# Optimization experiments

Hardware: AMD Instinct MI355X
Metric: run time of the kernel (lower is better)

The kernel has to match this reference:

```python
import jax, jax.numpy as jnp
import numpy as np

B, S, D, H = 1, 4096, 1024, 16
HD = D // H  # head_dim = 64
NEG = -1e9

def setup_inputs() -> dict:
    key = jax.random.key(0)
    ks = jax.random.split(key, 5)
    scale = 1.0 / np.sqrt(D)
    x = jax.random.normal(ks[0], (B, S, D), dtype=jnp.float32)
    Wq = jax.random.normal(ks[1], (D, D), dtype=jnp.float32) * scale
    Wk = jax.random.normal(ks[2], (D, D), dtype=jnp.float32) * scale
    Wv = jax.random.normal(ks[3], (D, D), dtype=jnp.float32) * scale
    Wo = jax.random.normal(ks[4], (D, D), dtype=jnp.float32) * scale
    mask = jnp.tril(jnp.ones((S, S), dtype=bool))[None, None]  # [1,1,S,S] causal
    return {"x": x, "mask": mask, "Wq": Wq, "Wk": Wk, "Wv": Wv, "Wo": Wo}

def reference(x, mask, Wq, Wk, Wv, Wo):
    # Linear projections (bias=False). nn.Linear computes x @ W.T; weights here
    # are stored as [out, in] so we use x @ W.T for faithfulness.
    q = x @ Wq.T  # [B,S,D]
    k = x @ Wk.T
    v = x @ Wv.T
    def split_heads(t):
        return t.reshape(B, S, H, HD).transpose(0, 2, 1, 3)  # [B,H,S,HD]
    q, k, v = split_heads(q), split_heads(k), split_heads(v)
    scores = jnp.einsum("bhqd,bhkd->bhqk", q, k) / jnp.sqrt(jnp.float32(HD))
    scores = jnp.where(mask, scores, NEG)
    attn = jax.nn.softmax(scores, axis=-1)  # dropout p=0.0 -> identity
    out = jnp.einsum("bhqk,bhkd->bhqd", attn, v)  # [B,H,S,HD]
    out = out.transpose(0, 2, 1, 3).reshape(B, S, D)
    return out @ Wo.T
```

## Files before the change

### kernel.cpp

```cpp
#include <hip/hip_runtime.h>
#include <hip/hip_bf16.h>


typedef __bf16 bf16x8 __attribute__((ext_vector_type(8)));
typedef __bf16 bf16x4 __attribute__((ext_vector_type(4)));
typedef float f32x4 __attribute__((ext_vector_type(4)));

#define GAS __attribute__((address_space(1)))
#define LAS __attribute__((address_space(3)))

__device__ __forceinline__ void async_copy16(const void* g, void* l) {
  __builtin_amdgcn_global_load_lds((const GAS unsigned int*)g,
                                   (LAS unsigned int*)l, 16, 0, 0);
}

__global__ __launch_bounds__(256) void cvt_all(const float* __restrict__ x,
                                               const float* __restrict__ Wq,
                                               const float* __restrict__ Wk,
                                               const float* __restrict__ Wv,
                                               const float* __restrict__ Wo,
                                               __bf16* __restrict__ xb,
                                               __bf16* __restrict__ Wc,
                                               __bf16* __restrict__ Wob) {
  int b = blockIdx.x;
  const float* src;
  __bf16* dst;
  if (b < 4096)      { src = x  + (b       ) * 1024; dst = xb  + (long)b * 1024; }
  else if (b < 5120) { src = Wq + (b - 4096) * 1024; dst = Wc  + (long)(b - 4096) * 1024; }
  else if (b < 6144) { src = Wk + (b - 5120) * 1024; dst = Wc  + (1l << 20) + (long)(b - 5120) * 1024; }
  else if (b < 7168) { src = Wv + (b - 6144) * 1024; dst = Wc  + (2l << 20) + (long)(b - 6144) * 1024; }
  else               { src = Wo + (b - 7168) * 1024; dst = Wob + (long)(b - 7168) * 1024; }
  int i = threadIdx.x * 4;
  float4 f = *(const float4*)(src + i);
  bf16x4 o;
  o[0] = (__bf16)f.x; o[1] = (__bf16)f.y; o[2] = (__bf16)f.z; o[3] = (__bf16)f.w;
  *(bf16x4*)(dst + i) = o;
}

__global__ __launch_bounds__(256) void gemm_qkv(const __bf16* __restrict__ A,
                                                const __bf16* __restrict__ B,
                                                __bf16* __restrict__ Qb,
                                                __bf16* __restrict__ Kf,
                                                __bf16* __restrict__ Vf) {
  const int K = 1024;
  __shared__ __bf16 As[128 * 32];
  __shared__ __bf16 Bs[128 * 32];
  const int tid = threadIdx.x;
  const int lane = tid & 63, wv = tid >> 6;
  const int l15 = lane & 15, quad = lane >> 4;
  const int wm = wv >> 1, wn = wv & 1;
  const int mbase = blockIdx.y * 128, nbase = blockIdx.x * 128;
  const bool kswap = (nbase >= 1024) && (nbase < 2048);

  f32x4 acc[4][4] = {};

  for (int k0 = 0; k0 < K; k0 += 32) {
    __syncthreads();
#pragma unroll
    for (int q = 0; q < 2; ++q) {
      int i = q * 256 + tid;
      int row = i >> 2, kg = i & 3;
      const __bf16* ga = A + (long)(mbase + row) * K + k0 + kg * 8;
      const __bf16* gb = B + (long)(nbase + row) * K + k0 + kg * 8;
      char* la = (char*)As + (q * 256 + wv * 64) * 16;
      char* lb = (char*)Bs + (q * 256 + wv * 64) * 16;
      async_copy16(ga, la);
      async_copy16(gb, lb);
    }
    __syncthreads();
    bf16x8 af[4], bfr[4];
#pragma unroll
    for (int i = 0; i < 4; ++i)
      af[i] = *(const bf16x8*)&As[(wm * 64 + i * 16 + l15) * 32 + quad * 8];
#pragma unroll
    for (int j = 0; j < 4; ++j)
      bfr[j] = *(const bf16x8*)&Bs[(wn * 64 + j * 16 + l15) * 32 + quad * 8];
    if (kswap) {
#pragma unroll
      for (int i = 0; i < 4; ++i)
#pragma unroll
        for (int j = 0; j < 4; ++j)
          acc[i][j] = __builtin_amdgcn_mfma_f32_16x16x32_bf16(bfr[j], af[i], acc[i][j], 0, 0, 0);
    } else {
#pragma unroll
      for (int i = 0; i < 4; ++i)
#pragma unroll
        for (int j = 0; j < 4; ++j)
          acc[i][j] = __builtin_amdgcn_mfma_f32_16x16x32_bf16(af[i], bfr[j], acc[i][j], 0, 0, 0);
    }
  }

  if (nbase < 1024) {
    const float QS = 0.18033688011112043f;
#pragma unroll
    for (int i = 0; i < 4; ++i)
#pragma unroll
      for (int j = 0; j < 4; ++j) {
        int col = nbase + wn * 64 + j * 16 + l15;
#pragma unroll
        for (int r = 0; r < 4; ++r) {
          int row = mbase + wm * 64 + i * 16 + quad * 4 + r;
          Qb[(long)row * 1024 + col] = (__bf16)(acc[i][j][r] * QS);
        }
      }
  } else if (nbase < 2048) {
#pragma unroll
    for (int i = 0; i < 4; ++i)
#pragma unroll
      for (int j = 0; j < 4; ++j) {
        int d0 = nbase - 1024 + wn * 64 + j * 16 + quad * 4;
        int h = d0 >> 6, dd = d0 & 63;
        int kk = dd >> 5, qf = (dd >> 3) & 3, e0 = dd & 7;
        int kt = mbase + wm * 64 + i * 16 + l15;
        int tile = kt >> 6;
        long off = ((long)(h * 64 + tile) * 8 + i * 2 + kk) * 512 + (qf * 16 + l15) * 8 + e0;
        union { __bf16 b[4]; uint2 u; } pk;
#pragma unroll
        for (int r = 0; r < 4; ++r) pk.b[r] = (__bf16)acc[i][j][r];
        *(uint2*)(Kf + off) = pk.u;
      }
  } else {
#pragma unroll
    for (int i = 0; i < 4; ++i)
#pragma unroll
      for (int j = 0; j < 4; ++j) {
        int col = nbase - 2048 + wn * 64 + j * 16 + l15;
        int h = col >> 6, dd = col & 63;
        int jd = dd >> 4, lv = dd & 15;
        int kt0 = mbase + wm * 64 + i * 16 + quad * 4;
        int tile = kt0 >> 6, w6 = kt0 & 63;
        int t = w6 >> 5, qv = (w6 >> 3) & 3, e0 = w6 & 7;
        long off = ((long)(h * 64 + tile) * 8 + jd * 2 + t) * 512 + (qv * 16 + lv) * 8 + e0;
        union { __bf16 b[4]; uint2 u; } pk;
#pragma unroll
        for (int r = 0; r < 4; ++r) pk.b[r] = (__bf16)acc[i][j][r];
        *(uint2*)(Vf + off) = pk.u;
      }
  }
}

__global__ __launch_bounds__(256) void gemm_wo(const __bf16* __restrict__ A,
                                               const __bf16* __restrict__ B,
                                               float* __restrict__ C) {
  const int K = 1024, N = 1024;
  __shared__ __bf16 As[128 * 32];
  __shared__ __bf16 Bs[64 * 32];
  const int tid = threadIdx.x;
  const int lane = tid & 63, wv = tid >> 6;
  const int l15 = lane & 15, quad = lane >> 4;
  const int wm = wv >> 1, wn = wv & 1;
  const int mbase = blockIdx.y * 128, nbase = blockIdx.x * 64;

  f32x4 acc[4][2] = {};

  for (int k0 = 0; k0 < K; k0 += 32) {
    __syncthreads();
#pragma unroll
    for (int q = 0; q < 2; ++q) {
      int i = q * 256 + tid;
      int row = i >> 2, kg = i & 3;
      const __bf16* ga = A + (long)(mbase + row) * K + k0 + kg * 8;
      char* la = (char*)As + (q * 256 + wv * 64) * 16;
      async_copy16(ga, la);
    }
    {
      int row = tid >> 2, kg = tid & 3;
      const __bf16* gb = B + (long)(nbase + row) * K + k0 + kg * 8;
      char* lb = (char*)Bs + (wv * 64) * 16;
      async_copy16(gb, lb);
    }
    __syncthreads();
    bf16x8 af[4], bfr[2];
#pragma unroll
    for (int i = 0; i < 4; ++i)
      af[i] = *(const bf16x8*)&As[(wm * 64 + i * 16 + l15) * 32 + quad * 8];
#pragma unroll
    for (int j = 0; j < 2; ++j)
      bfr[j] = *(const bf16x8*)&Bs[(wn * 32 + j * 16 + l15) * 32 + quad * 8];
#pragma unroll
    for (int i = 0; i < 4; ++i)
#pragma unroll
      for (int j = 0; j < 2; ++j)
        acc[i][j] = __builtin_amdgcn_mfma_f32_16x16x32_bf16(af[i], bfr[j], acc[i][j], 0, 0, 0);
  }
#pragma unroll
  for (int i = 0; i < 4; ++i)
#pragma unroll
    for (int j = 0; j < 2; ++j)
#pragma unroll
      for (int r = 0; r < 4; ++r) {
        int row = mbase + wm * 64 + i * 16 + quad * 4 + r;
        int col = nbase + wn * 32 + j * 16 + l15;
        C[(long)row * N + col] = acc[i][j][r];
      }
}

__global__ __launch_bounds__(256, 2) void flash_attn(const __bf16* __restrict__ Qb,
                                                     const __bf16* __restrict__ Kf,
                                                     const __bf16* __restrict__ Vf,
                                                     __bf16* __restrict__ AO) {
  __shared__ float Ms[2][64][36];
  const int tid = threadIdx.x;
  const int lane = tid & 63, l15 = lane & 15, quad = lane >> 4;
  const int w = tid >> 6;
  const int u = w >> 1, hf = w & 1;
  const int b = blockIdx.x;
  const int h = (b & 7) + 8 * ((b >> 3) & 1);
  const int T = 63 - (b >> 4);
  const int hoff = h * 64;

  const __bf16* Kh = Kf + (long)h * 64 * 4096;
  const __bf16* Vh = Vf + (long)h * 64 * 4096;

  bf16x8 qf[2][2];
#pragma unroll
  for (int g = 0; g < 2; ++g) {
    const int qrow = T * 64 + u * 32 + g * 16 + l15;
    qf[g][0] = *(const bf16x8*)(Qb + (long)qrow * 1024 + hoff + quad * 8);
    qf[g][1] = *(const bf16x8*)(Qb + (long)qrow * 1024 + hoff + 32 + quad * 8);
  }

  const int nkt = T + 1;
  const int kt0 = hf ? (nkt >> 1) : 0;
  const int kt1 = hf ? nkt : (nkt >> 1);
  f32x4 o_acc[2][4] = {};
  float l_acc[2] = {0.0f, 0.0f};

  bf16x8 kc[8];
  if (kt0 < kt1) {
    const __bf16* Kt = Kh + (long)kt0 * 4096;
#pragma unroll
    for (int f = 0; f < 8; ++f)
      kc[f] = *(const bf16x8*)(Kt + f * 512 + lane * 8);
  }

  for (int kt = kt0; kt < kt1; ++kt) {
    const __bf16* Vt = Vh + (long)kt * 4096;

    f32x4 stg[2][4] = {};
#pragma unroll
    for (int g = 0; g < 2; ++g)
#pragma unroll
      for (int j = 0; j < 4; ++j) {
        stg[g][j] = __builtin_amdgcn_mfma_f32_16x16x32_bf16(kc[j * 2 + 0], qf[g][0], stg[g][j], 0, 0, 0);
        stg[g][j] = __builtin_amdgcn_mfma_f32_16x16x32_bf16(kc[j * 2 + 1], qf[g][1], stg[g][j], 0, 0, 0);
      }

    bf16x8 va0[4];
#pragma unroll
    for (int jd = 0; jd < 4; ++jd)
      va0[jd] = *(const bf16x8*)(Vt + (jd * 2) * 512 + lane * 8);

    if (kt + 1 < kt1) {
      const __bf16* Kt = Kh + (long)(kt + 1) * 4096;
#pragma unroll
      for (int f = 0; f < 8; ++f)
        kc[f] = *(const bf16x8*)(Kt + f * 512 + lane * 8);
    }

    if (kt == nkt - 1) {
#pragma unroll
      for (int g = 0; g < 2; ++g) {
        const int dq = u * 32 + g * 16 + l15;
#pragma unroll
        for (int j = 0; j < 4; ++j)
#pragma unroll
          for (int r = 0; r < 4; ++r)
            if (j * 16 + quad * 4 + r > dq) stg[g][j][r] = -3.0e38f;
      }
    }

    unsigned dj[2][4][2];
#pragma unroll
    for (int g = 0; g < 2; ++g) {
      float ps = 0.0f;
#pragma unroll
      for (int j = 0; j < 4; ++j) {
        f32x4 pj;
#pragma unroll
        for (int r = 0; r < 4; ++r) pj[r] = __builtin_amdgcn_exp2f(stg[g][j][r]);
        ps += (pj[0] + pj[1]) + (pj[2] + pj[3]);
        union { __bf16 h2[2]; unsigned uu; } p0, p1;
        p0.h2[0] = (__bf16)pj[0]; p0.h2[1] = (__bf16)pj[1];
        p1.h2[0] = (__bf16)pj[2]; p1.h2[1] = (__bf16)pj[3];
        dj[g][j][0] = p0.uu;
        dj[g][j][1] = p1.uu;
      }
      l_acc[g] += ps;
    }

    bf16x8 va1[4];
#pragma unroll
    for (int jd = 0; jd < 4; ++jd)
      va1[jd] = *(const bf16x8*)(Vt + (jd * 2 + 1) * 512 + lane * 8);

#pragma unroll
    for (int g = 0; g < 2; ++g) {
      unsigned m0 = dj[g][0][0], m2 = dj[g][1][0];
      unsigned m1 = dj[g][0][1], m3 = dj[g][1][1];
      asm volatile("v_permlane32_swap_b32 %0, %1" : "+v"(m0), "+v"(m2));
      asm volatile("v_permlane32_swap_b32 %0, %1" : "+v"(m1), "+v"(m3));
      asm volatile("v_permlane16_swap_b32 %0, %1" : "+v"(m0), "+v"(m2));
      asm volatile("v_permlane16_swap_b32 %0, %1" : "+v"(m1), "+v"(m3));
      union { unsigned u4[4]; bf16x8 v; } Bf;
      Bf.u4[0] = m0; Bf.u4[1] = m1; Bf.u4[2] = m2; Bf.u4[3] = m3;
#pragma unroll
      for (int jd = 0; jd < 4; ++jd)
        o_acc[g][jd] = __builtin_amdgcn_mfma_f32_16x16x32_bf16(va0[jd], Bf.v, o_acc[g][jd], 0, 0, 0);
    }
#pragma unroll
    for (int g = 0; g < 2; ++g) {
      unsigned m0 = dj[g][2][0], m2 = dj[g][3][0];
      unsigned m1 = dj[g][2][1], m3 = dj[g][3][1];
      asm volatile("v_permlane32_swap_b32 %0, %1" : "+v"(m0), "+v"(m2));
      asm volatile("v_permlane32_swap_b32 %0, %1" : "+v"(m1), "+v"(m3));
      asm volatile("v_permlane16_swap_b32 %0, %1" : "+v"(m0), "+v"(m2));
      asm volatile("v_permlane16_swap_b32 %0, %1" : "+v"(m1), "+v"(m3));
      union { unsigned u4[4]; bf16x8 v; } Bf;
      Bf.u4[0] = m0; Bf.u4[1] = m1; Bf.u4[2] = m2; Bf.u4[3] = m3;
#pragma unroll
      for (int jd = 0; jd < 4; ++jd)
        o_acc[g][jd] = __builtin_amdgcn_mfma_f32_16x16x32_bf16(va1[jd], Bf.v, o_acc[g][jd], 0, 0, 0);
    }
  }

  if (hf) {
#pragma unroll
    for (int g = 0; g < 2; ++g)
#pragma unroll
      for (int jd = 0; jd < 4; ++jd)
        *(f32x4*)&Ms[u][lane][g * 16 + jd * 4] = o_acc[g][jd];
    Ms[u][lane][32] = l_acc[0];
    Ms[u][lane][33] = l_acc[1];
  }
  __syncthreads();
  if (!hf) {
#pragma unroll
    for (int g = 0; g < 2; ++g) {
      float la = l_acc[g];
#pragma unroll
      for (int jd = 0; jd < 4; ++jd)
        o_acc[g][jd] += *(const f32x4*)&Ms[u][lane][g * 16 + jd * 4];
      la += Ms[u][lane][32 + g];
      la += __shfl_xor(la, 16);
      la += __shfl_xor(la, 32);
      const float inv = 1.0f / la;
      const int qrow = T * 64 + u * 32 + g * 16 + l15;
#pragma unroll
      for (int jd = 0; jd < 4; ++jd) {
        bf16x4 ob;
#pragma unroll
        for (int r = 0; r < 4; ++r) ob[r] = (__bf16)(o_acc[g][jd][r] * inv);
        *(bf16x4*)(AO + (long)qrow * 1024 + hoff + jd * 16 + quad * 4) = ob;
      }
    }
  }
}

extern "C" void kernel_launch(void* const* d_in, const int* in_sizes, int n_in,
                              void* d_out, int out_size, void* d_ws, size_t ws_size,
                              hipStream_t stream) {
  const float* x  = (const float*)d_in[0];
  const float* Wq = (const float*)d_in[2];
  const float* Wk = (const float*)d_in[3];
  const float* Wv = (const float*)d_in[4];
  const float* Wo = (const float*)d_in[5];
  float* out = (float*)d_out;

  char* ws = (char*)d_ws;
  __bf16* xb  = (__bf16*)ws;
  __bf16* Wc  = (__bf16*)(ws + (8u << 20));
  __bf16* Wob = (__bf16*)(ws + (14u << 20));
  __bf16* Qb  = (__bf16*)(ws + (16u << 20));
  __bf16* Kfr = (__bf16*)(ws + (24u << 20));
  __bf16* Vfr = (__bf16*)(ws + (32u << 20));
  __bf16* AO  = (__bf16*)(ws + (40u << 20));

  cvt_all<<<8192, 256, 0, stream>>>(x, Wq, Wk, Wv, Wo, xb, Wc, Wob);

  dim3 g1(3072 / 128, 4096 / 128);
  gemm_qkv<<<g1, 256, 0, stream>>>(xb, Wc, Qb, Kfr, Vfr);

  flash_attn<<<1024, 256, 0, stream>>>(Qb, Kfr, Vfr, AO);

  dim3 g2(1024 / 64, 4096 / 128);
  gemm_wo<<<g2, 256, 0, stream>>>(AO, Wob, out);
}
```

Measured before the change: 233.8 us.

## Pair causal query tiles per block and split keys four ways per tile

Each block now handles two query tiles, P and 63-P, one after the other, so every block does the same amount of causal work. Blocks grow to 512 threads with 8 waves, and each query half splits its key range across four waves instead of two. Partial outputs and row sums are reduced through a larger shared-memory buffer. This should remove tail imbalance from uneven causal blocks. In exchange, grid parallelism halves and each pass adds a barrier and a bigger reduction.

```diff
diff --git a/kernel.cpp b/kernel.cpp
--- a/kernel.cpp
+++ b/kernel.cpp
@@ -195,165 +195,172 @@
       }
 }
 
-__global__ __launch_bounds__(256, 2) void flash_attn(const __bf16* __restrict__ Qb,
+__global__ __launch_bounds__(512, 2) void flash_attn(const __bf16* __restrict__ Qb,
                                                      const __bf16* __restrict__ Kf,
                                                      const __bf16* __restrict__ Vf,
                                                      __bf16* __restrict__ AO) {
-  __shared__ float Ms[2][64][36];
+  __shared__ float Ms[2][3][64][36];
   const int tid = threadIdx.x;
   const int lane = tid & 63, l15 = lane & 15, quad = lane >> 4;
   const int w = tid >> 6;
-  const int u = w >> 1, hf = w & 1;
+  const int u = w >> 2, qtr = w & 3;
   const int b = blockIdx.x;
   const int h = (b & 7) + 8 * ((b >> 3) & 1);
-  const int T = 63 - (b >> 4);
+  const int P = b >> 4;
   const int hoff = h * 64;
 
   const __bf16* Kh = Kf + (long)h * 64 * 4096;
   const __bf16* Vh = Vf + (long)h * 64 * 4096;
 
-  bf16x8 qf[2][2];
-#pragma unroll
-  for (int g = 0; g < 2; ++g) {
-    const int qrow = T * 64 + u * 32 + g * 16 + l15;
-    qf[g][0] = *(const bf16x8*)(Qb + (long)qrow * 1024 + hoff + quad * 8);
-    qf[g][1] = *(const bf16x8*)(Qb + (long)qrow * 1024 + hoff + 32 + quad * 8);
-  }
-
-  const int nkt = T + 1;
-  const int kt0 = hf ? (nkt >> 1) : 0;
-  const int kt1 = hf ? nkt : (nkt >> 1);
-  f32x4 o_acc[2][4] = {};
-  float l_acc[2] = {0.0f, 0.0f};
-
-  bf16x8 kc[8];
-  if (kt0 < kt1) {
-    const __bf16* Kt = Kh + (long)kt0 * 4096;
-#pragma unroll
-    for (int f = 0; f < 8; ++f)
-      kc[f] = *(const bf16x8*)(Kt + f * 512 + lane * 8);
-  }
-
-  for (int kt = kt0; kt < kt1; ++kt) {
-    const __bf16* Vt = Vh + (long)kt * 4096;
-
-    f32x4 stg[2][4] = {};
-#pragma unroll
-    for (int g = 0; g < 2; ++g)
-#pragma unroll
-      for (int j = 0; j < 4; ++j) {
-        stg[g][j] = __builtin_amdgcn_mfma_f32_16x16x32_bf16(kc[j * 2 + 0], qf[g][0], stg[g][j], 0, 0, 0);
-        stg[g][j] = __builtin_amdgcn_mfma_f32_16x16x32_bf16(kc[j * 2 + 1], qf[g][1], stg[g][j], 0, 0, 0);
-      }
-
-    bf16x8 va0[4];
-#pragma unroll
-    for (int jd = 0; jd < 4; ++jd)
-      va0[jd] = *(const bf16x8*)(Vt + (jd * 2) * 512 + lane * 8);
-
-    if (kt + 1 < kt1) {
-      const __bf16* Kt = Kh + (long)(kt + 1) * 4096;
+  for (int pass = 0; pass < 2; ++pass) {
+    const int T = pass ? (63 - P) : P;
+    bf16x8 qf[2][2];
+#pragma unroll
+    for (int g = 0; g < 2; ++g) {
+      const int qrow = T * 64 + u * 32 + g * 16 + l15;
+      qf[g][0] = *(const bf16x8*)(Qb + (long)qrow * 1024 + hoff + quad * 8);
+      qf[g][1] = *(const bf16x8*)(Qb + (long)qrow * 1024 + hoff + 32 + quad * 8);
+    }
+
+    const int nkt = T + 1;
+    const int kt0 = (nkt * qtr) >> 2;
+    const int kt1 = (nkt * (qtr + 1)) >> 2;
+    f32x4 o_acc[2][4] = {};
+    float l_acc[2] = {0.0f, 0.0f};
+
+    bf16x8 kc[8];
+    if (kt0 < kt1) {
+      const __bf16* Kt = Kh + (long)kt0 * 4096;
 #pragma unroll
       for (int f = 0; f < 8; ++f)
         kc[f] = *(const bf16x8*)(Kt + f * 512 + lane * 8);
     }
 
-    if (kt == nkt - 1) {
+    for (int kt = kt0; kt < kt1; ++kt) {
+      const __bf16* Vt = Vh + (long)kt * 4096;
+
+      f32x4 stg[2][4] = {};
+#pragma unroll
+      for (int g = 0; g < 2; ++g)
+#pragma unroll
+        for (int j = 0; j < 4; ++j) {
+          stg[g][j] = __builtin_amdgcn_mfma_f32_16x16x32_bf16(kc[j * 2 + 0], qf[g][0], stg[g][j], 0, 0, 0);
+          stg[g][j] = __builtin_amdgcn_mfma_f32_16x16x32_bf16(kc[j * 2 + 1], qf[g][1], stg[g][j], 0, 0, 0);
+        }
+
+      bf16x8 va0[4];
+#pragma unroll
+      for (int jd = 0; jd < 4; ++jd)
+        va0[jd] = *(const bf16x8*)(Vt + (jd * 2) * 512 + lane * 8);
+
+      if (kt + 1 < kt1) {
+        const __bf16* Kt = Kh + (long)(kt + 1) * 4096;
+#pragma unroll
+        for (int f = 0; f < 8; ++f)
+          kc[f] = *(const bf16x8*)(Kt + f * 512 + lane * 8);
+      }
+
+      if (kt == nkt - 1) {
+#pragma unroll
+        for (int g = 0; g < 2; ++g) {
+          const int dq = u * 32 + g * 16 + l15;
+#pragma unroll
+          for (int j = 0; j < 4; ++j)
+#pragma unroll
+            for (int r = 0; r < 4; ++r)
+              if (j * 16 + quad * 4 + r > dq) stg[g][j][r] = -3.0e38f;
+        }
+      }
+
+      unsigned dj[2][4][2];
 #pragma unroll
       for (int g = 0; g < 2; ++g) {
-        const int dq = u * 32 + g * 16 + l15;
-#pragma unroll
-        for (int j = 0; j < 4; ++j)
-#pragma unroll
-          for (int r = 0; r < 4; ++r)
-            if (j * 16 + quad * 4 + r > dq) stg[g][j][r] = -3.0e38f;
-      }
-    }
-
-    unsigned dj[2][4][2];
-#pragma unroll
-    for (int g = 0; g < 2; ++g) {
-      float ps = 0.0f;
-#pragma unroll
-      for (int j = 0; j < 4; ++j) {
-        f32x4 pj;
-#pragma unroll
-        for (int r = 0; r < 4; ++r) pj[r] = __builtin_amdgcn_exp2f(stg[g][j][r]);
-        ps += (pj[0] + pj[1]) + (pj[2] + pj[3]);
-        union { __bf16 h2[2]; unsigned uu; } p0, p1;
-        p0.h2[0] = (__bf16)pj[0]; p0.h2[1] = (__bf16)pj[1];
-        p1.h2[0] = (__bf16)pj[2]; p1.h2[1] = (__bf16)pj[3];
-        dj[g][j][0] = p0.uu;
-        dj[g][j][1] = p1.uu;
-      }
-      l_acc[g] += ps;
-    }
-
-    bf16x8 va1[4];
-#pragma unroll
-    for (int jd = 0; jd < 4; ++jd)
-      va1[jd] = *(const bf16x8*)(Vt + (jd * 2 + 1) * 512 + lane * 8);
-
-#pragma unroll
-    for (int g = 0; g < 2; ++g) {
-      unsigned m0 = dj[g][0][0], m2 = dj[g][1][0];
-      unsigned m1 = dj[g][0][1], m3 = dj[g][1][1];
-      asm volatile("v_permlane32_swap_b32 %0, %1" : "+v"(m0), "+v"(m2));
-      asm volatile("v_permlane32_swap_b32 %0, %1" : "+v"(m1), "+v"(m3));
-      asm volatile("v_permlane16_swap_b32 %0, %1" : "+v"(m0), "+v"(m2));
-      asm volatile("v_permlane16_swap_b32 %0, %1" : "+v"(m1), "+v"(m3));
-      union { unsigned u4[4]; bf16x8 v; } Bf;
-      Bf.u4[0] = m0; Bf.u4[1] = m1; Bf.u4[2] = m2; Bf.u4[3] = m3;
+        float ps = 0.0f;
+#pragma unroll
+        for (int j = 0; j < 4; ++j) {
+          f32x4 pj;
+#pragma unroll
+          for (int r = 0; r < 4; ++r) pj[r] = __builtin_amdgcn_exp2f(stg[g][j][r]);
+          ps += (pj[0] + pj[1]) + (pj[2] + pj[3]);
+          union { __bf16 h2[2]; unsigned uu; } p0, p1;
+          p0.h2[0] = (__bf16)pj[0]; p0.h2[1] = (__bf16)pj[1];
+          p1.h2[0] = (__bf16)pj[2]; p1.h2[1] = (__bf16)pj[3];
+          dj[g][j][0] = p0.uu;
+          dj[g][j][1] = p1.uu;
+        }
+        l_acc[g] += ps;
+      }
+
+      bf16x8 va1[4];
 #pragma unroll
       for (int jd = 0; jd < 4; ++jd)
-        o_acc[g][jd] = __builtin_amdgcn_mfma_f32_16x16x32_bf16(va0[jd], Bf.v, o_acc[g][jd], 0, 0, 0);
-    }
-#pragma unroll
-    for (int g = 0; g < 2; ++g) {
-      unsigned m0 = dj[g][2][0], m2 = dj[g][3][0];
-      unsigned m1 = dj[g][2][1], m3 = dj[g][3][1];
-      asm volatile("v_permlane32_swap_b32 %0, %1" : "+v"(m0), "+v"(m2));
-      asm volatile("v_permlane32_swap_b32 %0, %1" : "+v"(m1), "+v"(m3));
-      asm volatile("v_permlane16_swap_b32 %0, %1" : "+v"(m0), "+v"(m2));
-      asm volatile("v_permlane16_swap_b32 %0, %1" : "+v"(m1), "+v"(m3));
-      union { unsigned u4[4]; bf16x8 v; } Bf;
-      Bf.u4[0] = m0; Bf.u4[1] = m1; Bf.u4[2] = m2; Bf.u4[3] = m3;
-#pragma unroll
-      for (int jd = 0; jd < 4; ++jd)
-        o_acc[g][jd] = __builtin_amdgcn_mfma_f32_16x16x32_bf16(va1[jd], Bf.v, o_acc[g][jd], 0, 0, 0);
-    }
-  }
-
-  if (hf) {
-#pragma unroll
-    for (int g = 0; g < 2; ++g)
-#pragma unroll
-      for (int jd = 0; jd < 4; ++jd)
-        *(f32x4*)&Ms[u][lane][g * 16 + jd * 4] = o_acc[g][jd];
-    Ms[u][lane][32] = l_acc[0];
-    Ms[u][lane][33] = l_acc[1];
-  }
-  __syncthreads();
-  if (!hf) {
-#pragma unroll
-    for (int g = 0; g < 2; ++g) {
-      float la = l_acc[g];
-#pragma unroll
-      for (int jd = 0; jd < 4; ++jd)
-        o_acc[g][jd] += *(const f32x4*)&Ms[u][lane][g * 16 + jd * 4];
-      la += Ms[u][lane][32 + g];
-      la += __shfl_xor(la, 16);
-      la += __shfl_xor(la, 32);
-      const float inv = 1.0f / la;
-      const int qrow = T * 64 + u * 32 + g * 16 + l15;
-#pragma unroll
-      for (int jd = 0; jd < 4; ++jd) {
-        bf16x4 ob;
-#pragma unroll
-        for (int r = 0; r < 4; ++r) ob[r] = (__bf16)(o_acc[g][jd][r] * inv);
-        *(bf16x4*)(AO + (long)qrow * 1024 + hoff + jd * 16 + quad * 4) = ob;
-      }
-    }
+        va1[jd] = *(const bf16x8*)(Vt + (jd * 2 + 1) * 512 + lane * 8);
+
+#pragma unroll
+      for (int g = 0; g < 2; ++g) {
+        unsigned m0 = dj[g][0][0], m2 = dj[g][1][0];
+        unsigned m1 = dj[g][0][1], m3 = dj[g][1][1];
+        asm volatile("v_permlane32_swap_b32 %0, %1" : "+v"(m0), "+v"(m2));
+        asm volatile("v_permlane32_swap_b32 %0, %1" : "+v"(m1), "+v"(m3));
+        asm volatile("v_permlane16_swap_b32 %0, %1" : "+v"(m0), "+v"(m2));
+        asm volatile("v_permlane16_swap_b32 %0, %1" : "+v"(m1), "+v"(m3));
+        union { unsigned u4[4]; bf16x8 v; } Bf;
+        Bf.u4[0] = m0; Bf.u4[1] = m1; Bf.u4[2] = m2; Bf.u4[3] = m3;
+#pragma unroll
+        for (int jd = 0; jd < 4; ++jd)
+          o_acc[g][jd] = __builtin_amdgcn_mfma_f32_16x16x32_bf16(va0[jd], Bf.v, o_acc[g][jd], 0, 0, 0);
+      }
+#pragma unroll
+      for (int g = 0; g < 2; ++g) {
+        unsigned m0 = dj[g][2][0], m2 = dj[g][3][0];
+        unsigned m1 = dj[g][2][1], m3 = dj[g][3][1];
+        asm volatile("v_permlane32_swap_b32 %0, %1" : "+v"(m0), "+v"(m2));
+        asm volatile("v_permlane32_swap_b32 %0, %1" : "+v"(m1), "+v"(m3));
+        asm volatile("v_permlane16_swap_b32 %0, %1" : "+v"(m0), "+v"(m2));
+        asm volatile("v_permlane16_swap_b32 %0, %1" : "+v"(m1), "+v"(m3));
+        union { unsigned u4[4]; bf16x8 v; } Bf;
+        Bf.u4[0] = m0; Bf.u4[1] = m1; Bf.u4[2] = m2; Bf.u4[3] = m3;
+#pragma unroll
+        for (int jd = 0; jd < 4; ++jd)
+          o_acc[g][jd] = __builtin_amdgcn_mfma_f32_16x16x32_bf16(va1[jd], Bf.v, o_acc[g][jd], 0, 0, 0);
+      }
+    }
+
+    if (qtr) {
+#pragma unroll
+      for (int g = 0; g < 2; ++g)
+#pragma unroll
+        for (int jd = 0; jd < 4; ++jd)
+          *(f32x4*)&Ms[u][qtr - 1][lane][g * 16 + jd * 4] = o_acc[g][jd];
+      Ms[u][qtr - 1][lane][32] = l_acc[0];
+      Ms[u][qtr - 1][lane][33] = l_acc[1];
+    }
+    __syncthreads();
+    if (!qtr) {
+#pragma unroll
+      for (int g = 0; g < 2; ++g) {
+        float la = l_acc[g];
+#pragma unroll
+        for (int sct = 0; sct < 3; ++sct) {
+#pragma unroll
+          for (int jd = 0; jd < 4; ++jd)
+            o_acc[g][jd] += *(const f32x4*)&Ms[u][sct][lane][g * 16 + jd * 4];
+          la += Ms[u][sct][lane][32 + g];
+        }
+        la += __shfl_xor(la, 16);
+        la += __shfl_xor(la, 32);
+        const float inv = 1.0f / la;
+        const int qrow = T * 64 + u * 32 + g * 16 + l15;
+#pragma unroll
+        for (int jd = 0; jd < 4; ++jd) {
+          bf16x4 ob;
+#pragma unroll
+          for (int r = 0; r < 4; ++r) ob[r] = (__bf16)(o_acc[g][jd][r] * inv);
+          *(bf16x4*)(AO + (long)qrow * 1024 + hoff + jd * 16 + quad * 4) = ob;
+        }
+      }
+    }
+    __syncthreads();
   }
 }
 
@@ -381,7 +388,7 @@
   dim3 g1(3072 / 128, 4096 / 128);
   gemm_qkv<<<g1, 256, 0, stream>>>(xb, Wc, Qb, Kfr, Vfr);
 
-  flash_attn<<<1024, 256, 0, stream>>>(Qb, Kfr, Vfr, AO);
+  flash_attn<<<512, 512, 0, stream>>>(Qb, Kfr, Vfr, AO);
 
   dim3 g2(1024 / 64, 4096 / 128);
   gemm_wo<<<g2, 256, 0, stream>>>(AO, Wob, out);
```

New measurement: 240.2 us. 2.7% more time.
